# Optimization experiments

Hardware: AMD Instinct MI355X
Metric: run time of the kernel (lower is better)

Reference implementation:

```python
import jax, jax.numpy as jnp
import numpy as np

DIM = 256
HEADS = 8
WS = 8
N = WS * WS
HID = 1024
EPS = 1e-5


def _rel_pos_index():
    ch, cw = np.meshgrid(np.arange(WS), np.arange(WS), indexing='ij')
    coords = np.stack([ch.ravel(), cw.ravel()])  # [2, N]
    rel = coords[:, :, None] - coords[:, None, :]  # [2, N, N]
    rel = rel.transpose(1, 2, 0).astype(np.int64)
    rel[:, :, 0] += WS - 1
    rel[:, :, 1] += WS - 1
    rel[:, :, 0] *= 2 * WS - 1
    return jnp.asarray(rel.sum(-1))  # [N, N]

REL_IDX = _rel_pos_index()


def layer_norm(x, g, b):
    mu = jnp.mean(x, axis=-1, keepdims=True)
    var = jnp.mean(jnp.square(x - mu), axis=-1, keepdims=True)
    return (x - mu) * jax.lax.rsqrt(var + EPS) * g + b


def setup_inputs() -> dict:
    key = jax.random.key(0)
    ks = jax.random.split(key, 12)
    s = 0.02
    return {
        'x': jax.random.normal(ks[0], (32, 4096, DIM), jnp.float32),
        'attn_mask': jnp.zeros((64, N, N), jnp.float32),  # unused (forward sets mask=None)
        'g1': jnp.ones((DIM,), jnp.float32),
        'b1': jnp.zeros((DIM,), jnp.float32),
        'w_qkv': jax.random.normal(ks[1], (3 * DIM, DIM), jnp.float32) * s,
        'b_qkv': jnp.zeros((3 * DIM,), jnp.float32),
        'bias_table': jax.random.normal(ks[2], ((2 * WS - 1) ** 2, HEADS), jnp.float32) * s,
        'w_proj': jax.random.normal(ks[3], (DIM, DIM), jnp.float32) * s,
        'b_proj': jnp.zeros((DIM,), jnp.float32),
        'g2': jnp.ones((DIM,), jnp.float32),
        'b2': jnp.zeros((DIM,), jnp.float32),
        'w_fc1': jax.random.normal(ks[4], (HID, DIM), jnp.float32) * s,
        'b_fc1': jnp.zeros((HID,), jnp.float32),
        'w_fc2': jax.random.normal(ks[5], (DIM, HID), jnp.float32) * s,
        'b_fc2': jnp.zeros((DIM,), jnp.float32),
    }


def reference(x, attn_mask, g1, b1, w_qkv, b_qkv, bias_table, w_proj, b_proj,
              g2, b2, w_fc1, b_fc1, w_fc2, b_fc2):
    B, L, C = x.shape
    H = W = int(np.sqrt(L))
    hd = C // HEADS
    scale = hd ** -0.5

    shortcut = x
    xn = layer_norm(x, g1, b1).reshape(B, H, W, C)
    xw = xn.reshape(B, H // WS, WS, W // WS, WS, C)
    xw = xw.transpose(0, 1, 3, 2, 4, 5).reshape(-1, N, C)  # [B_, N, C]

    qkv = (xw @ w_qkv.T + b_qkv).reshape(-1, N, 3, HEADS, hd)
    q, k, v = [qkv[:, :, i].transpose(0, 2, 1, 3) for i in range(3)]  # [B_, h, N, d]
    attn = jnp.einsum('bhnd,bhmd->bhnm', q * scale, k)
    bias = bias_table[REL_IDX]  # [N, N, h]
    attn = attn + bias.transpose(2, 0, 1)[None]
    attn = jax.nn.softmax(attn, axis=-1)
    out = jnp.einsum('bhnm,bhmd->bhnd', attn, v)
    out = out.transpose(0, 2, 1, 3).reshape(-1, N, C)
    out = out @ w_proj.T + b_proj

    # window reverse
    out = out.reshape(B, H // WS, W // WS, WS, WS, C)
    out = out.transpose(0, 1, 3, 2, 4, 5).reshape(B, L, C)

    x1 = shortcut + out
    h = layer_norm(x1, g2, b2) @ w_fc1.T + b_fc1
    h = jax.nn.gelu(h, approximate=False)
    return x1 + (h @ w_fc2.T + b_fc2)
```

## Files before the change

### kernel.cpp

```cpp
#include <hip/hip_runtime.h>
#include <hip/hip_bf16.h>
#include <hip/hip_fp16.h>

typedef _Float16 f16;
typedef __attribute__((ext_vector_type(8))) _Float16 f16x8;
typedef __attribute__((ext_vector_type(4))) _Float16 f16x4;
typedef __attribute__((ext_vector_type(2))) _Float16 f16x2;
typedef __attribute__((ext_vector_type(4))) float f32x4;

#define AS1(p) ((const __attribute__((address_space(1))) void*)(p))
#define AS3(p) ((__attribute__((address_space(3))) void*)(p))

__global__ __launch_bounds__(256) void cvt_weights(
    const float* __restrict__ wq, const float* __restrict__ wp,
    const float* __restrict__ wf1, const float* __restrict__ wf2,
    f16* __restrict__ o) {
  int i = blockIdx.x * 256 + threadIdx.x;
  float v;
  if (i < 196608)       v = wq[i];
  else if (i < 262144)  v = wp[i - 196608];
  else if (i < 524288)  v = wf1[i - 262144];
  else                  v = wf2[i - 524288];
  o[i] = (f16)v;
}

__global__ __launch_bounds__(256) void prep_bias(
    const float* __restrict__ bt, float* __restrict__ T) {
  const int flat = blockIdx.x * 256 + threadIdx.x;
  const int h = flat >> 12, l = (flat >> 6) & 63, s = flat & 63;
  const int i = s >> 4, j = (s >> 2) & 3, r = s & 3;
  const int n = 16 * i + 4 * (l >> 4) + r;
  const int m = 16 * j + (l & 15);
  const int idx = ((n >> 3) - (m >> 3) + 7) * 15 + ((n & 7) - (m & 7) + 7);
  T[flat] = bt[idx * 8 + h] * 1.4426950408889634f;
}

template<bool PART, typename TIN>
__global__ __launch_bounds__(256) void ln_rows(
    const TIN* __restrict__ x, const float* __restrict__ g,
    const float* __restrict__ b, f16* __restrict__ out) {
  const int t = blockIdx.x * 4 + (threadIdx.x >> 6);
  const int lane = threadIdx.x & 63;
  float v0, v1, v2, v3;
  if constexpr (sizeof(TIN) == 4) {
    const float4 v = ((const float4*)(x + (long)t * 256))[lane];
    v0 = v.x; v1 = v.y; v2 = v.z; v3 = v.w;
  } else {
    const f16x4 v = ((const f16x4*)(x + (long)t * 256))[lane];
    v0 = (float)v[0]; v1 = (float)v[1]; v2 = (float)v[2]; v3 = (float)v[3];
  }
  float s  = v0 + v1 + v2 + v3;
  float ss = v0*v0 + v1*v1 + v2*v2 + v3*v3;
  #pragma unroll
  for (int off = 32; off; off >>= 1) {
    s  += __shfl_xor(s, off);
    ss += __shfl_xor(ss, off);
  }
  const float mu = s * (1.0f / 256.0f);
  const float var = ss * (1.0f / 256.0f) - mu * mu;
  const float rs = rsqrtf(var + 1e-5f);
  const float4 gv = ((const float4*)g)[lane];
  const float4 bv = ((const float4*)b)[lane];
  long row;
  if (PART) {
    const int bI = t >> 12, l = t & 4095;
    const int hh = l >> 6, w2 = l & 63;
    const int wi = bI * 64 + (hh >> 3) * 8 + (w2 >> 3);
    const int n  = (hh & 7) * 8 + (w2 & 7);
    row = (long)wi * 64 + n;
  } else {
    row = t;
  }
  f16x4 o4;
  o4[0] = (f16)((v0 - mu) * rs * gv.x + bv.x);
  o4[1] = (f16)((v1 - mu) * rs * gv.y + bv.y);
  o4[2] = (f16)((v2 - mu) * rs * gv.z + bv.z);
  o4[3] = (f16)((v3 - mu) * rs * gv.w + bv.w);
  *(f16x4*)(out + row * 256 + lane * 4) = o4;
}

template<int EPI, int K>
__global__ __launch_bounds__(256) void gemm_bt(
    const f16* __restrict__ A, const f16* __restrict__ Bw,
    const float* __restrict__ bias, const float* __restrict__ residf,
    const f16* __restrict__ residh,
    f16* __restrict__ outh, float* __restrict__ outf, int N) {
  __shared__ f16 As[2][128 * 32];
  __shared__ f16 Bs[2][128 * 32];
  const int tid  = threadIdx.x;
  const int wid  = tid >> 6;
  const int lane = tid & 63;
  const int qd   = lane >> 4;
  const int l16  = lane & 15;
  const int gx  = gridDim.x;
  const int nwg = gx * gridDim.y;
  const int g   = blockIdx.y * gx + blockIdx.x;
  const int gs  = (g & 7) * (nwg >> 3) + (g >> 3);
  const long tM = (long)(gs / gx) * 128;
  const int  tN = (gs % gx) * 128;
  const int srow = lane >> 2;
  const int scol = ((lane & 3) ^ ((srow >> 1) & 3)) * 8;
  const int wm = (wid >> 1) * 64;
  const int wn = (wid & 1) * 64;
  const int rsw = (l16 >> 1) & 3;

  f32x4 acc[4][4];
  #pragma unroll
  for (int i = 0; i < 4; ++i)
    #pragma unroll
    for (int j = 0; j < 4; ++j) acc[i][j] = (f32x4){0.f, 0.f, 0.f, 0.f};

  const int nt = K / 32;

  #pragma unroll
  for (int t = 0; t < 2; ++t) {
    const int gidx = wid * 2 + t;
    const int row  = gidx * 16 + srow;
    __builtin_amdgcn_global_load_lds(AS1(A + (tM + row) * K + scol),
                                     AS3(&As[0][gidx * 512]), 16, 0, 0);
    __builtin_amdgcn_global_load_lds(AS1(Bw + (long)(tN + row) * K + scol),
                                     AS3(&Bs[0][gidx * 512]), 16, 0, 0);
  }
  asm volatile("s_waitcnt vmcnt(0)" ::: "memory");
  __builtin_amdgcn_s_barrier();

  int cur = 0;
  for (int t = 0; t < nt; ++t) {
    if (t + 1 < nt) {
      const int k0 = (t + 1) * 32;
      #pragma unroll
      for (int u = 0; u < 2; ++u) {
        const int gidx = wid * 2 + u;
        const int row  = gidx * 16 + srow;
        __builtin_amdgcn_global_load_lds(AS1(A + (tM + row) * K + k0 + scol),
                                         AS3(&As[cur ^ 1][gidx * 512]), 16, 0, 0);
        __builtin_amdgcn_global_load_lds(AS1(Bw + (long)(tN + row) * K + k0 + scol),
                                         AS3(&Bs[cur ^ 1][gidx * 512]), 16, 0, 0);
      }
    }
    f16x8 af[4], bf[4];
    #pragma unroll
    for (int i = 0; i < 4; ++i)
      af[i] = *(const f16x8*)&As[cur][(wm + i * 16 + l16) * 32 + ((qd ^ rsw) * 8)];
    #pragma unroll
    for (int j = 0; j < 4; ++j)
      bf[j] = *(const f16x8*)&Bs[cur][(wn + j * 16 + l16) * 32 + ((qd ^ rsw) * 8)];
    #pragma unroll
    for (int i = 0; i < 4; ++i)
      #pragma unroll
      for (int j = 0; j < 4; ++j)
        acc[i][j] = __builtin_amdgcn_mfma_f32_16x16x32_f16(af[i], bf[j], acc[i][j], 0, 0, 0);
    asm volatile("s_waitcnt vmcnt(0)" ::: "memory");
    __builtin_amdgcn_s_barrier();
    cur ^= 1;
  }

  float bb[4];
  #pragma unroll
  for (int j = 0; j < 4; ++j) bb[j] = bias[tN + wn + j * 16 + l16];

  if (EPI == 3) {
    #pragma unroll
    for (int j = 0; j < 4; ++j) {
      const int col = tN + wn + j * 16 + l16;
      #pragma unroll
      for (int i = 0; i < 4; ++i) {
        #pragma unroll
        for (int r = 0; r < 4; ++r) {
          const long row = tM + wm + i * 16 + qd * 4 + r;
          const long off = row * 256 + col;
          outf[off] = (float)residh[off] + acc[i][j][r] + bb[j];
        }
      }
    }
  } else {
    f16* slice = &As[0][0] + wid * 1024;
    const int rrow = lane >> 3;
    const int seg  = lane & 7;
    #pragma unroll
    for (int i = 0; i < 4; ++i) {
      #pragma unroll
      for (int j = 0; j < 4; ++j) {
        #pragma unroll
        for (int r = 0; r < 4; ++r) {
          float v = acc[i][j][r] + bb[j];
          if (EPI == 2) v = 0.5f * v * (1.0f + erff(v * 0.70710678118654752f));
          const int r16 = qd * 4 + r;
          slice[r16 * 64 + ((j * 16 + l16) ^ ((r16 & 7) << 3))] = (f16)v;
        }
      }
      __syncthreads();
      #pragma unroll
      for (int hrow = 0; hrow < 16; hrow += 8) {
        const int lrow = hrow + rrow;
        const f16x8 v8 = *(const f16x8*)(slice + lrow * 64 + (seg ^ (lrow & 7)) * 8);
        const long grow = tM + wm + i * 16 + lrow;
        const int  gc   = tN + wn + seg * 8;
        if (EPI == 1) {
          const int rw = (int)grow;
          const int wi = rw >> 6, n = rw & 63;
          const int bI = wi >> 6, wloc = wi & 63;
          const int hh = (wloc >> 3) * 8 + (n >> 3);
          const int w2 = (wloc & 7) * 8 + (n & 7);
          const long prow = (long)bI * 4096 + hh * 64 + w2;
          const float* rp = residf + prow * 256 + gc;
          f16x8 o;
          #pragma unroll
          for (int k = 0; k < 8; ++k) o[k] = (f16)(rp[k] + (float)v8[k]);
          *(f16x8*)(outh + prow * 256 + gc) = o;
        } else {
          *(f16x8*)(outh + grow * N + gc) = v8;
        }
      }
      __syncthreads();
    }
  }
}

__global__ __launch_bounds__(256, 3) void attn_win(
    const f16* __restrict__ qkv, const float* __restrict__ bt,
    f16* __restrict__ out) {
  __shared__ __align__(16) char SMEM[4 * 12800];
  const int wid = threadIdx.x >> 6, lane = threadIdx.x & 63;
  const int qd = lane >> 4, l16 = lane & 15;
  const int unit = blockIdx.x * 4 + wid;
  const int wi = unit >> 3, h = unit & 7;
  char* W = SMEM + wid * 12800;
  f16* VT = (f16*)W;
  char* Pb = W + 4608;

  const f16* qbase = qkv + (long)wi * 64 * 768 + h * 32;

  f16x8 qa[4], kb[4];
  #pragma unroll
  for (int i = 0; i < 4; ++i)
    qa[i] = *(const f16x8*)(qbase + (16 * i + l16) * 768 + qd * 8);
  #pragma unroll
  for (int j = 0; j < 4; ++j)
    kb[j] = *(const f16x8*)(qbase + 256 + (16 * j + l16) * 768 + qd * 8);

  #pragma unroll
  for (int it = 0; it < 4; ++it) {
    const f16x8 v8 = *(const f16x8*)(qbase + 512 + (16 * it + l16) * 768 + qd * 8);
    #pragma unroll
    for (int e = 0; e < 8; ++e)
      VT[(qd * 8 + e) * 72 + 16 * it + l16] = v8[e];
  }

  f32x4 S[4][4];
  #pragma unroll
  for (int i = 0; i < 4; ++i)
    #pragma unroll
    for (int j = 0; j < 4; ++j) S[i][j] = (f32x4){0.f, 0.f, 0.f, 0.f};
  #pragma unroll
  for (int i = 0; i < 4; ++i)
    #pragma unroll
    for (int j = 0; j < 4; ++j)
      S[i][j] = __builtin_amdgcn_mfma_f32_16x16x32_f16(qa[i], kb[j], S[i][j], 0, 0, 0);

  const float SC = 0.17677669529663687f * 1.4426950408889634f;
  const float* Tb = bt + ((h * 64 + lane) << 6);
  #pragma unroll
  for (int i = 0; i < 4; ++i) {
    f32x4 b0 = *(const f32x4*)(Tb + i * 16);
    f32x4 b1 = *(const f32x4*)(Tb + i * 16 + 4);
    f32x4 b2 = *(const f32x4*)(Tb + i * 16 + 8);
    f32x4 b3 = *(const f32x4*)(Tb + i * 16 + 12);
    #pragma unroll
    for (int r = 0; r < 4; ++r) {
      S[i][0][r] = S[i][0][r] * SC + b0[r];
      S[i][1][r] = S[i][1][r] * SC + b1[r];
      S[i][2][r] = S[i][2][r] * SC + b2[r];
      S[i][3][r] = S[i][3][r] * SC + b3[r];
    }
  }

  float inv[4][4];
  #pragma unroll
  for (int i = 0; i < 4; ++i) {
    #pragma unroll
    for (int r = 0; r < 4; ++r) {
      float mx = fmaxf(fmaxf(S[i][0][r], S[i][1][r]), fmaxf(S[i][2][r], S[i][3][r]));
      #pragma unroll
      for (int msk = 1; msk < 16; msk <<= 1) mx = fmaxf(mx, __shfl_xor(mx, msk));
      float s0 = 0.f;
      #pragma unroll
      for (int j = 0; j < 4; ++j) {
        const float p = __builtin_amdgcn_exp2f(S[i][j][r] - mx);
        S[i][j][r] = p;
        s0 += p;
      }
      #pragma unroll
      for (int msk = 1; msk < 16; msk <<= 1) s0 += __shfl_xor(s0, msk);
      inv[i][r] = __builtin_amdgcn_rcpf(s0);
    }
  }

  #pragma unroll
  for (int i = 0; i < 4; ++i) {
    #pragma unroll
    for (int r = 0; r < 4; ++r) {
      const int n = 16 * i + 4 * qd + r;
      char* rowp = Pb + n * 128;
      const int sw = (n & 7) << 4;
      #pragma unroll
      for (int j = 0; j < 4; ++j)
        *(f16*)(rowp + ((j * 32 + l16 * 2) ^ sw)) = (f16)S[i][j][r];
    }
  }

  f32x4 O[4][2];
  #pragma unroll
  for (int i = 0; i < 4; ++i) {
    O[i][0] = (f32x4){0.f, 0.f, 0.f, 0.f};
    O[i][1] = (f32x4){0.f, 0.f, 0.f, 0.f};
  }
  #pragma unroll
  for (int kk = 0; kk < 2; ++kk) {
    f16x8 vb[2];
    #pragma unroll
    for (int jj = 0; jj < 2; ++jj)
      vb[jj] = *(const f16x8*)((const char*)W + (16 * jj + l16) * 144 + kk * 64 + qd * 16);
    #pragma unroll
    for (int i = 0; i < 4; ++i) {
      const f16x8 pa = *(const f16x8*)(Pb + (16 * i + l16) * 128 +
                                       ((kk * 64 + qd * 16) ^ ((l16 & 7) << 4)));
      #pragma unroll
      for (int jj = 0; jj < 2; ++jj)
        O[i][jj] = __builtin_amdgcn_mfma_f32_16x16x32_f16(pa, vb[jj], O[i][jj], 0, 0, 0);
    }
  }

  #pragma unroll
  for (int i = 0; i < 4; ++i) {
    #pragma unroll
    for (int jj = 0; jj < 2; ++jj) {
      #pragma unroll
      for (int r = 0; r < 4; ++r) {
        const int n = 16 * i + 4 * qd + r;
        *(f16*)(Pb + n * 80 + jj * 32 + l16 * 2) = (f16)(O[i][jj][r] * inv[i][r]);
      }
    }
  }
  #pragma unroll
  for (int it = 0; it < 4; ++it) {
    const int row = 16 * it + l16;
    const f16x8 o8 = *(const f16x8*)(Pb + row * 80 + qd * 16);
    *(f16x8*)(out + ((long)wi * 64 + row) * 256 + h * 32 + qd * 8) = o8;
  }
}

extern "C" void kernel_launch(void* const* d_in, const int* in_sizes, int n_in,
                              void* d_out, int out_size, void* d_ws, size_t ws_size,
                              hipStream_t stream) {
  const float* x     = (const float*)d_in[0];
  const float* g1    = (const float*)d_in[2];
  const float* b1    = (const float*)d_in[3];
  const float* wqkv  = (const float*)d_in[4];
  const float* bqkv  = (const float*)d_in[5];
  const float* btab  = (const float*)d_in[6];
  const float* wproj = (const float*)d_in[7];
  const float* bproj = (const float*)d_in[8];
  const float* g2    = (const float*)d_in[9];
  const float* b2    = (const float*)d_in[10];
  const float* wfc1  = (const float*)d_in[11];
  const float* bfc1  = (const float*)d_in[12];
  const float* wfc2  = (const float*)d_in[13];
  const float* bfc2  = (const float*)d_in[14];
  float* out = (float*)d_out;

  char* ws = (char*)d_ws;
  f16* wgt   = (f16*)ws;
  f16* wq16  = wgt;
  f16* wp16  = wgt + 196608;
  f16* wf116 = wgt + 262144;
  f16* wf216 = wgt + 524288;
  float* Tbuf = (float*)(ws + 1572864);

  int CH = 1;
  for (int cand = 32; cand >= 1; cand >>= 1) {
    const size_t need = 2097152ULL + (size_t)cand * 12582912ULL;
    if (need <= ws_size) { CH = cand; break; }
  }
  const int NC = 32 / CH;

  const size_t O_xn  = 2097152ULL;
  const size_t O_qkv = O_xn  + (size_t)CH * 2097152ULL;
  const size_t O_x1  = O_qkv + (size_t)CH * 6291456ULL;
  const size_t O_xn2 = O_x1  + (size_t)CH * 2097152ULL;
  f16* xnw  = (f16*)(ws + O_xn);
  f16* qkvb = (f16*)(ws + O_qkv);
  f16* x1h  = (f16*)(ws + O_x1);
  f16* xn2  = (f16*)(ws + O_xn2);
  f16* hbuf = (f16*)(ws + O_xn);

  cvt_weights<<<3072, 256, 0, stream>>>(wqkv, wproj, wfc1, wfc2, wgt);
  prep_bias<<<128, 256, 0, stream>>>(btab, Tbuf);

  const long imgElems = 4096L * 256;
  for (int c = 0; c < NC; ++c) {
    const float* xc  = x   + (long)c * CH * imgElems;
    float*       oc  = out + (long)c * CH * imgElems;
    ln_rows<true, float><<<CH * 1024, 256, 0, stream>>>(xc, g1, b1, xnw);
    gemm_bt<0, 256><<<dim3(6, CH * 32), 256, 0, stream>>>(xnw, wq16, bqkv, nullptr, nullptr, qkvb, nullptr, 768);
    attn_win<<<CH * 128, 256, 0, stream>>>(qkvb, Tbuf, xnw);
    gemm_bt<1, 256><<<dim3(2, CH * 32), 256, 0, stream>>>(xnw, wp16, bproj, xc, nullptr, x1h, nullptr, 256);
    ln_rows<false, f16><<<CH * 1024, 256, 0, stream>>>(x1h, g2, b2, xn2);
    gemm_bt<2, 256><<<dim3(8, CH * 32), 256, 0, stream>>>(xn2, wf116, bfc1, nullptr, nullptr, hbuf, nullptr, 1024);
    gemm_bt<3, 1024><<<dim3(2, CH * 32), 256, 0, stream>>>(hbuf, wf216, bfc2, nullptr, x1h, nullptr, oc, 256);
  }
}
```

Measured before the change: 801.7 us.

## Prefetch GEMM tiles two stages ahead and use fast GELU approximation

Restructures the GEMM main loop so global-to-LDS loads for tile t+2 are issued after fragments of tile t are read into registers, with a partial vmcnt wait, letting loads overlap more MFMA work. It also replaces the erf-based GELU with a sigmoid-style tanh approximation computed with exp2 and rcp intrinsics, which removes the cost of erff. The loop assumes nt is at least 2 and that the final buffers are indices 0 and 1, which holds only when nt is even. The GELU approximation changes numerics slightly compared with the exact erf form.

```diff
diff --git a/kernel.cpp b/kernel.cpp
--- a/kernel.cpp
+++ b/kernel.cpp
@@ -111,49 +111,58 @@
     for (int j = 0; j < 4; ++j) acc[i][j] = (f32x4){0.f, 0.f, 0.f, 0.f};
 
   const int nt = K / 32;
-
-  #pragma unroll
-  for (int t = 0; t < 2; ++t) {
-    const int gidx = wid * 2 + t;
-    const int row  = gidx * 16 + srow;
-    __builtin_amdgcn_global_load_lds(AS1(A + (tM + row) * K + scol),
-                                     AS3(&As[0][gidx * 512]), 16, 0, 0);
-    __builtin_amdgcn_global_load_lds(AS1(Bw + (long)(tN + row) * K + scol),
-                                     AS3(&Bs[0][gidx * 512]), 16, 0, 0);
-  }
+  f16x8 af[4], bf[4];
+
+  auto stage_tile = [&](int tt) {
+    const int k0 = tt * 32;
+    f16* Ad = &As[tt & 1][0];
+    f16* Bd = &Bs[tt & 1][0];
+    #pragma unroll
+    for (int u = 0; u < 2; ++u) {
+      const int gidx = wid * 2 + u;
+      const int row  = gidx * 16 + srow;
+      __builtin_amdgcn_global_load_lds(AS1(A + (tM + row) * K + k0 + scol),
+                                       AS3(&Ad[gidx * 512]), 16, 0, 0);
+      __builtin_amdgcn_global_load_lds(AS1(Bw + (long)(tN + row) * K + k0 + scol),
+                                       AS3(&Bd[gidx * 512]), 16, 0, 0);
+    }
+  };
+  auto load_frags = [&](int cb) {
+    #pragma unroll
+    for (int i = 0; i < 4; ++i)
+      af[i] = *(const f16x8*)&As[cb][(wm + i * 16 + l16) * 32 + ((qd ^ rsw) * 8)];
+    #pragma unroll
+    for (int j = 0; j < 4; ++j)
+      bf[j] = *(const f16x8*)&Bs[cb][(wn + j * 16 + l16) * 32 + ((qd ^ rsw) * 8)];
+  };
+  auto do_mfma = [&]() {
+    #pragma unroll
+    for (int i = 0; i < 4; ++i)
+      #pragma unroll
+      for (int j = 0; j < 4; ++j)
+        acc[i][j] = __builtin_amdgcn_mfma_f32_16x16x32_f16(af[i], bf[j], acc[i][j], 0, 0, 0);
+  };
+
+  stage_tile(0);
+  stage_tile(1);
+
+  for (int t = 0; t < nt - 2; ++t) {
+    asm volatile("s_waitcnt vmcnt(4)" ::: "memory");
+    __builtin_amdgcn_s_barrier();
+    load_frags(t & 1);
+    asm volatile("s_waitcnt lgkmcnt(0)" ::: "memory");
+    __builtin_amdgcn_s_barrier();
+    stage_tile(t + 2);
+    do_mfma();
+  }
+  asm volatile("s_waitcnt vmcnt(4)" ::: "memory");
+  __builtin_amdgcn_s_barrier();
+  load_frags(0);
+  do_mfma();
   asm volatile("s_waitcnt vmcnt(0)" ::: "memory");
   __builtin_amdgcn_s_barrier();
-
-  int cur = 0;
-  for (int t = 0; t < nt; ++t) {
-    if (t + 1 < nt) {
-      const int k0 = (t + 1) * 32;
-      #pragma unroll
-      for (int u = 0; u < 2; ++u) {
-        const int gidx = wid * 2 + u;
-        const int row  = gidx * 16 + srow;
-        __builtin_amdgcn_global_load_lds(AS1(A + (tM + row) * K + k0 + scol),
-                                         AS3(&As[cur ^ 1][gidx * 512]), 16, 0, 0);
-        __builtin_amdgcn_global_load_lds(AS1(Bw + (long)(tN + row) * K + k0 + scol),
-                                         AS3(&Bs[cur ^ 1][gidx * 512]), 16, 0, 0);
-      }
-    }
-    f16x8 af[4], bf[4];
-    #pragma unroll
-    for (int i = 0; i < 4; ++i)
-      af[i] = *(const f16x8*)&As[cur][(wm + i * 16 + l16) * 32 + ((qd ^ rsw) * 8)];
-    #pragma unroll
-    for (int j = 0; j < 4; ++j)
-      bf[j] = *(const f16x8*)&Bs[cur][(wn + j * 16 + l16) * 32 + ((qd ^ rsw) * 8)];
-    #pragma unroll
-    for (int i = 0; i < 4; ++i)
-      #pragma unroll
-      for (int j = 0; j < 4; ++j)
-        acc[i][j] = __builtin_amdgcn_mfma_f32_16x16x32_f16(af[i], bf[j], acc[i][j], 0, 0, 0);
-    asm volatile("s_waitcnt vmcnt(0)" ::: "memory");
-    __builtin_amdgcn_s_barrier();
-    cur ^= 1;
-  }
+  load_frags(1);
+  do_mfma();
 
   float bb[4];
   #pragma unroll
@@ -184,7 +193,12 @@
         #pragma unroll
         for (int r = 0; r < 4; ++r) {
           float v = acc[i][j][r] + bb[j];
-          if (EPI == 2) v = 0.5f * v * (1.0f + erff(v * 0.70710678118654752f));
+          if (EPI == 2) {
+            const float u2 = v * v;
+            const float w  = v * (-2.3022082f - 0.10294324f * u2);
+            const float e  = __builtin_amdgcn_exp2f(w);
+            v = v * __builtin_amdgcn_rcpf(1.0f + e);
+          }
           const int r16 = qd * 4 + r;
           slice[r16 * 64 + ((j * 16 + l16) ^ ((r16 & 7) << 3))] = (f16)v;
         }
```

Result: faster. 781.2 us (-2.5%).
